# Kernel optimization log

Hardware: AMD Instinct MI355X
Metric: run time of the kernel (lower is better)

Reference implementation:

```python
import jax, jax.numpy as jnp
import numpy as np

N_NODES = 50000


def sage_conv(x, src, dst, Wl, bl, Wr):
    # mean-aggregate neighbor features: message from src -> dst
    msg = x[src]                                            # [E, d]
    agg = jax.ops.segment_sum(msg, dst, num_segments=N_NODES)
    deg = jax.ops.segment_sum(jnp.ones((src.shape[0],), x.dtype), dst,
                              num_segments=N_NODES)
    mean = agg / jnp.clip(deg, 1.0)[:, None]                # [N, d]
    # PyG SAGEConv: lin_l(mean) + lin_r(x); lin_l has bias, lin_r does not
    return mean @ Wl.T + bl + x @ Wr.T


def setup_inputs() -> dict:
    key = jax.random.key(0)
    ks = jax.random.split(key, 10)
    d_in, d_h = 128, 256
    E = 800000
    x = jax.random.normal(ks[0], (N_NODES, d_in), jnp.float32)
    edge_index = jax.random.randint(ks[1], (2, E), 0, N_NODES, jnp.int32)
    s = 0.05
    return {
        "x": x,
        "edge_index": edge_index,
        "W1_l": jax.random.normal(ks[2], (d_h, d_in), jnp.float32) * s,
        "b1": jax.random.normal(ks[3], (d_h,), jnp.float32) * s,
        "W1_r": jax.random.normal(ks[4], (d_h, d_in), jnp.float32) * s,
        "W2_l": jax.random.normal(ks[5], (d_h, d_h), jnp.float32) * s,
        "b2": jax.random.normal(ks[6], (d_h,), jnp.float32) * s,
        "W2_r": jax.random.normal(ks[7], (d_h, d_h), jnp.float32) * s,
        "head_w": jax.random.normal(ks[8], (1, d_h), jnp.float32) * s,
        "head_b": jax.random.normal(ks[9], (1,), jnp.float32) * s,
    }


def reference(x, edge_index, W1_l, b1, W1_r, W2_l, b2, W2_r, head_w, head_b):
    src, dst = edge_index[0], edge_index[1]
    h = jax.nn.relu(sage_conv(x, src, dst, W1_l, b1, W1_r))
    # dropout is identity in eval mode
    h = jax.nn.relu(sage_conv(h, src, dst, W2_l, b2, W2_r))
    out = h @ head_w.T + head_b                              # [N, 1]
    return out[:, 0]                                         # [N]
```

## Files before the change

kernel.cpp:

```cpp
#include <hip/hip_runtime.h>
#include <hip/hip_bf16.h>
#include <hip/hip_fp8.h>

#define D_IN 128
#define D_H  256
#define NBLK 128
#define BSH  7
#define BNODES 128

typedef __attribute__((ext_vector_type(8))) short short8;
typedef __attribute__((ext_vector_type(4))) float floatx4;

__device__ __forceinline__ unsigned short f2bf(float f) {
    __hip_bfloat16 h = __float2bfloat16(f);
    return *reinterpret_cast<unsigned short*>(&h);
}
__device__ __forceinline__ float bf2f(unsigned short s) {
    union { unsigned int u; float f; } v;
    v.u = ((unsigned int)s) << 16;
    return v.f;
}
__device__ __forceinline__ unsigned char f2fp8(float f) {
    __hip_fp8_e4m3 t(f);
    return (unsigned char)t.__x;
}

__global__ void p1_hist_conv_k(const int* __restrict__ dst, int* __restrict__ cnt2d,
                               int E, int NB,
                               const float* __restrict__ x, unsigned short* __restrict__ xb,
                               unsigned char* __restrict__ xb8, int nx4,
                               const float* __restrict__ w1l, unsigned short* __restrict__ w1lb,
                               const float* __restrict__ w1r, unsigned short* __restrict__ w1rb, int nw14,
                               const float* __restrict__ w2l, unsigned short* __restrict__ w2lb,
                               const float* __restrict__ w2r, unsigned short* __restrict__ w2rb, int nw24) {
    if (blockIdx.x < NBLK) {
        __shared__ int h[512];
        for (int i = threadIdx.x; i < NB; i += 256) h[i] = 0;
        __syncthreads();
        for (int e = blockIdx.x * 256 + threadIdx.x; e < E; e += NBLK * 256)
            atomicAdd(&h[dst[e] >> BSH], 1);
        __syncthreads();
        for (int i = threadIdx.x; i < NB; i += 256)
            cnt2d[blockIdx.x * NB + i] = h[i];
        return;
    }
    int i = (blockIdx.x - NBLK) * 256 + threadIdx.x;
    if (i < nx4) {
        float4 v = ((const float4*)x)[i];
        ushort4 u;
        u.x = f2bf(v.x); u.y = f2bf(v.y); u.z = f2bf(v.z); u.w = f2bf(v.w);
        ((ushort4*)xb)[i] = u;
        uchar4 c;
        c.x = f2fp8(v.x); c.y = f2fp8(v.y); c.z = f2fp8(v.z); c.w = f2fp8(v.w);
        ((uchar4*)xb8)[i] = c;
        return;
    }
    i -= nx4;
    const float* s; unsigned short* d; int k;
    if (i < nw14) { s = w1l; d = w1lb; k = i; }
    else {
        i -= nw14;
        if (i < nw14) { s = w1r; d = w1rb; k = i; }
        else {
            i -= nw14;
            if (i < nw24) { s = w2l; d = w2lb; k = i; }
            else {
                i -= nw24;
                if (i >= nw24) return;
                s = w2r; d = w2rb; k = i;
            }
        }
    }
    float4 v = ((const float4*)s)[k];
    ushort4 u;
    u.x = f2bf(v.x); u.y = f2bf(v.y); u.z = f2bf(v.z); u.w = f2bf(v.w);
    ((ushort4*)d)[k] = u;
}

__global__ __launch_bounds__(NBLK) void bucket_scan_k(const int* __restrict__ cnt2d,
                                                      int* __restrict__ off2d,
                                                      int* __restrict__ tot, int NB) {
    const int B = blockIdx.x, t = threadIdx.x;
    __shared__ int sc[NBLK];
    __shared__ int orig[NBLK];
    int v = cnt2d[t * NB + B];
    orig[t] = v; sc[t] = v;
    __syncthreads();
    for (int off = 1; off < NBLK; off <<= 1) {
        int u = (t >= off) ? sc[t - off] : 0;
        __syncthreads();
        sc[t] += u;
        __syncthreads();
    }
    off2d[t * NB + B] = sc[t] - orig[t];
    if (t == NBLK - 1) tot[B] = sc[t];
}

__global__ __launch_bounds__(512) void base_scan_k(const int* __restrict__ tot,
                                                   int* __restrict__ base,
                                                   int* __restrict__ rp,
                                                   int NB, int M, int E) {
    __shared__ int sc[512];
    const int t = threadIdx.x;
    int v = (t < NB) ? tot[t] : 0;
    sc[t] = v;
    __syncthreads();
    for (int off = 1; off < 512; off <<= 1) {
        int u = (t >= off) ? sc[t - off] : 0;
        __syncthreads();
        sc[t] += u;
        __syncthreads();
    }
    if (t < NB) base[t] = sc[t] - v;
    if (t == NB - 1) base[NB] = sc[t];
    if (t == 0) rp[M] = E;
}

__global__ __launch_bounds__(256) void place_k(const int* __restrict__ src,
                                               const int* __restrict__ dst,
                                               const int* __restrict__ off2d,
                                               const int* __restrict__ base,
                                               unsigned int* __restrict__ staging,
                                               int E, int NB) {
    __shared__ int cur[512];
    const int b = blockIdx.x;
    for (int i = threadIdx.x; i < NB; i += 256)
        cur[i] = base[i] + off2d[b * NB + i];
    __syncthreads();
    for (int e = b * 256 + threadIdx.x; e < E; e += NBLK * 256) {
        const int d = dst[e];
        const int pos = atomicAdd(&cur[d >> BSH], 1);
        staging[pos] = ((unsigned int)(d & (BNODES - 1)) << 16) | (unsigned int)src[e];
    }
}

__global__ __launch_bounds__(256) void bucket_sort_k(const unsigned int* __restrict__ staging,
                                                     const int* __restrict__ base,
                                                     int* __restrict__ rp, int* __restrict__ col,
                                                     int M) {
    const int B = blockIdx.x, tid = threadIdx.x;
    __shared__ int h[BNODES], sc[BNODES], cur[BNODES];
    if (tid < BNODES) h[tid] = 0;
    __syncthreads();
    const int s0 = base[B], s1 = base[B + 1];
    for (int i = s0 + tid; i < s1; i += 256)
        atomicAdd(&h[staging[i] >> 16], 1);
    __syncthreads();
    if (tid < BNODES) sc[tid] = h[tid];
    __syncthreads();
    for (int off = 1; off < BNODES; off <<= 1) {
        int v = 0;
        if (tid < BNODES && tid >= off) v = sc[tid - off];
        __syncthreads();
        if (tid < BNODES) sc[tid] += v;
        __syncthreads();
    }
    if (tid < BNODES) {
        const int excl = sc[tid] - h[tid];
        const int node = B * BNODES + tid;
        if (node < M) rp[node] = s0 + excl;
        cur[tid] = s0 + excl;
    }
    __syncthreads();
    for (int i = s0 + tid; i < s1; i += 256) {
        const unsigned int u = staging[i];
        const int pos = atomicAdd(&cur[u >> 16], 1);
        col[pos] = (int)(u & 0xFFFFu);
    }
}

template <int UNP>
__device__ __forceinline__ int agg1_stage(const unsigned char* __restrict__ X8,
                                          const int* __restrict__ col,
                                          int j, int e, int sel, int l32, float* acc) {
    for (; j + 2 * UNP <= e; j += 2 * UNP) {
        int c0[UNP], c1[UNP];
#pragma unroll
        for (int u = 0; u < UNP; ++u) { c0[u] = col[j + 2 * u]; c1[u] = col[j + 2 * u + 1]; }
        unsigned int vals[UNP];
#pragma unroll
        for (int u = 0; u < UNP; ++u) {
            const int cs = sel ? c1[u] : c0[u];
            vals[u] = *(const unsigned int*)(X8 + (size_t)cs * 128 + l32 * 4);
        }
#pragma unroll
        for (int u = 0; u < UNP; ++u) {
            __hip_fp8x4_e4m3 p;
            p.__x = vals[u];
            float4 f = (float4)p;
            acc[0] += f.x; acc[1] += f.y; acc[2] += f.z; acc[3] += f.w;
        }
    }
    return j;
}

__global__ __launch_bounds__(256) void aggregate1_k(
    const unsigned char* __restrict__ X8, const int* __restrict__ col,
    const int* __restrict__ rp, unsigned short* __restrict__ out, int Mnodes) {
    int node = __builtin_amdgcn_readfirstlane((blockIdx.x << 2) + (threadIdx.x >> 6));
    if (node >= Mnodes) return;
    const int lane = threadIdx.x & 63;
    const int sel = lane >> 5;
    const int l32 = lane & 31;
    const int s = rp[node], e = rp[node + 1];
    float acc[4] = {0.f, 0.f, 0.f, 0.f};

    int j = s;
    j = agg1_stage<4>(X8, col, j, e, sel, l32, acc);
    j = agg1_stage<2>(X8, col, j, e, sel, l32, acc);
    j = agg1_stage<1>(X8, col, j, e, sel, l32, acc);
    if (j < e) {
        const int c0 = col[j];
        if (sel == 0) {
            unsigned int v = *(const unsigned int*)(X8 + (size_t)c0 * 128 + l32 * 4);
            __hip_fp8x4_e4m3 p;
            p.__x = v;
            float4 f = (float4)p;
            acc[0] += f.x; acc[1] += f.y; acc[2] += f.z; acc[3] += f.w;
        }
    }
#pragma unroll
    for (int k = 0; k < 4; ++k) acc[k] += __shfl_xor(acc[k], 32, 64);
    const float inv = 1.f / fmaxf((float)(e - s), 1.f);
    if (sel == 0) {
        ushort4 o;
        o.x = f2bf(acc[0] * inv); o.y = f2bf(acc[1] * inv);
        o.z = f2bf(acc[2] * inv); o.w = f2bf(acc[3] * inv);
        *(ushort4*)(out + (size_t)node * 128 + l32 * 4) = o;
    }
}

template <int UN>
__device__ __forceinline__ int agg_stage_fp8(const unsigned char* __restrict__ X8,
                                             const int* __restrict__ col,
                                             int j, int e, int lane, float* acc) {
    for (; j + UN <= e; j += UN) {
        int cs[UN];
#pragma unroll
        for (int u = 0; u < UN; ++u) cs[u] = col[j + u];
        unsigned int vals[UN];
#pragma unroll
        for (int u = 0; u < UN; ++u)
            vals[u] = *(const unsigned int*)(X8 + (size_t)cs[u] * 256 + lane * 4);
#pragma unroll
        for (int u = 0; u < UN; ++u) {
            __hip_fp8x4_e4m3 p;
            p.__x = vals[u];
            float4 f = (float4)p;
            acc[0] += f.x; acc[1] += f.y; acc[2] += f.z; acc[3] += f.w;
        }
    }
    return j;
}

__global__ __launch_bounds__(256) void aggregate2_k(
    const unsigned char* __restrict__ X8, const int* __restrict__ col,
    const int* __restrict__ rp, unsigned short* __restrict__ out, int Mnodes) {
    int node = __builtin_amdgcn_readfirstlane((blockIdx.x << 2) + (threadIdx.x >> 6));
    if (node >= Mnodes) return;
    const int lane = threadIdx.x & 63;
    const int s = rp[node], e = rp[node + 1];
    float acc[4] = {0.f, 0.f, 0.f, 0.f};

    int j = s;
    j = agg_stage_fp8<8>(X8, col, j, e, lane, acc);
    j = agg_stage_fp8<4>(X8, col, j, e, lane, acc);
    j = agg_stage_fp8<2>(X8, col, j, e, lane, acc);
    j = agg_stage_fp8<1>(X8, col, j, e, lane, acc);

    const float inv = 1.f / fmaxf((float)(e - s), 1.f);
    ushort4 o;
    o.x = f2bf(acc[0] * inv); o.y = f2bf(acc[1] * inv);
    o.z = f2bf(acc[2] * inv); o.w = f2bf(acc[3] * inv);
    *(ushort4*)(out + (size_t)node * 256 + lane * 4) = o;
}

template <int K, bool HEAD>
__global__ __launch_bounds__(256, 2) void gemm_mfma_k(
    const unsigned short* __restrict__ A1, const unsigned short* __restrict__ W1,
    const unsigned short* __restrict__ A2, const unsigned short* __restrict__ W2,
    const float* __restrict__ bias, unsigned short* __restrict__ Hout,
    unsigned char* __restrict__ Hout8,
    const float* __restrict__ hw, const float* __restrict__ hb,
    float* __restrict__ out, int M) {
    __shared__ __align__(16) unsigned short sA[128 * 40];
    __shared__ __align__(16) unsigned short sB[256 * 40];
    __shared__ float head_acc[128];

    constexpr int NCK = K / 32;
    constexpr int NC = 2 * NCK;

    const int tid = threadIdx.x;
    const int wave = tid >> 6;
    const int lane = tid & 63;
    const int c = lane & 15;
    const int q = lane >> 4;
    const int m0 = blockIdx.x * 128;

    if (HEAD && tid < 128) head_acc[tid] = 0.f;

    floatx4 acc[8][4];
#pragma unroll
    for (int mi = 0; mi < 8; ++mi)
#pragma unroll
        for (int ni = 0; ni < 4; ++ni) acc[mi][ni] = (floatx4){0.f, 0.f, 0.f, 0.f};

    const int arow = tid >> 1;
    const int aseg = (tid & 1) * 16;
    const int brow = tid >> 2;
    const int bseg = (tid & 3) * 8;
    int gr = m0 + arow;
    if (gr >= M) gr = M - 1;

    auto loadChunk = [&](int t, short8& a0, short8& a1, short8* b) {
        const unsigned short* Ap = (t >= NCK) ? A2 : A1;
        const unsigned short* Wp = (t >= NCK) ? W2 : W1;
        const int k0 = (t & (NCK - 1)) * 32;
        a0 = *(const short8*)(Ap + (size_t)gr * K + k0 + aseg);
        a1 = *(const short8*)(Ap + (size_t)gr * K + k0 + aseg + 8);
#pragma unroll
        for (int i = 0; i < 4; ++i)
            b[i] = *(const short8*)(Wp + (size_t)(brow + i * 64) * K + k0 + bseg);
    };

    short8 ca0, ca1, cb[4], na0, na1, nb[4];
    loadChunk(0, ca0, ca1, cb);

#pragma unroll 1
    for (int t = 0; t < NC; ++t) {
        __syncthreads();
        *(short8*)&sA[arow * 40 + aseg] = ca0;
        *(short8*)&sA[arow * 40 + aseg + 8] = ca1;
#pragma unroll
        for (int i = 0; i < 4; ++i)
            *(short8*)&sB[(brow + i * 64) * 40 + bseg] = cb[i];
        if (t + 1 < NC)
            loadChunk(t + 1, na0, na1, nb);
        __syncthreads();

        short8 af[8], bf[4];
#pragma unroll
        for (int mi = 0; mi < 8; ++mi)
            af[mi] = *(const short8*)&sA[(mi * 16 + c) * 40 + q * 8];
#pragma unroll
        for (int ni = 0; ni < 4; ++ni)
            bf[ni] = *(const short8*)&sB[(wave * 64 + ni * 16 + c) * 40 + q * 8];
#pragma unroll
        for (int mi = 0; mi < 8; ++mi)
#pragma unroll
            for (int ni = 0; ni < 4; ++ni)
                acc[mi][ni] = __builtin_amdgcn_mfma_f32_16x16x32_bf16(
                    af[mi], bf[ni], acc[mi][ni], 0, 0, 0);

        ca0 = na0; ca1 = na1;
#pragma unroll
        for (int i = 0; i < 4; ++i) cb[i] = nb[i];
    }

    if (!HEAD) {
#pragma unroll
        for (int mi = 0; mi < 8; ++mi)
#pragma unroll
            for (int ni = 0; ni < 4; ++ni) {
                const int n = wave * 64 + ni * 16 + c;
                const float bv = bias[n];
#pragma unroll
                for (int reg = 0; reg < 4; ++reg) {
                    const int m = m0 + mi * 16 + q * 4 + reg;
                    if (m < M) {
                        float v = fmaxf(acc[mi][ni][reg] + bv, 0.f);
                        Hout[(size_t)m * 256 + n] = f2bf(v);
                        Hout8[(size_t)m * 256 + n] = f2fp8(v);
                    }
                }
            }
    } else {
#pragma unroll
        for (int mi = 0; mi < 8; ++mi) {
            float p[4] = {0.f, 0.f, 0.f, 0.f};
#pragma unroll
            for (int ni = 0; ni < 4; ++ni) {
                const int n = wave * 64 + ni * 16 + c;
                const float bv = bias[n];
                const float hv = hw[n];
#pragma unroll
                for (int reg = 0; reg < 4; ++reg)
                    p[reg] += fmaxf(acc[mi][ni][reg] + bv, 0.f) * hv;
            }
#pragma unroll
            for (int reg = 0; reg < 4; ++reg) {
                float v = p[reg];
                v += __shfl_xor(v, 1, 64);
                v += __shfl_xor(v, 2, 64);
                v += __shfl_xor(v, 4, 64);
                v += __shfl_xor(v, 8, 64);
                if (c == 0) atomicAdd(&head_acc[mi * 16 + q * 4 + reg], v);
            }
        }
        __syncthreads();
        if (tid < 128) {
            const int m = m0 + tid;
            if (m < M) out[m] = head_acc[tid] + hb[0];
        }
    }
}

extern "C" void kernel_launch(void* const* d_in, const int* in_sizes, int n_in,
                              void* d_out, int out_size, void* d_ws, size_t ws_size,
                              hipStream_t stream) {
    const float* x    = (const float*)d_in[0];
    const int*   ei   = (const int*)d_in[1];
    const float* W1l  = (const float*)d_in[2];
    const float* b1   = (const float*)d_in[3];
    const float* W1r  = (const float*)d_in[4];
    const float* W2l  = (const float*)d_in[5];
    const float* b2   = (const float*)d_in[6];
    const float* W2r  = (const float*)d_in[7];
    const float* hw   = (const float*)d_in[8];
    const float* hb   = (const float*)d_in[9];
    float* out = (float*)d_out;

    const int M = in_sizes[0] / D_IN;
    const int E = in_sizes[1] / 2;
    const int* src = ei;
    const int* dst = ei + E;
    const int NB = (M + BNODES - 1) / BNODES;

    size_t off = 0;
    auto alloc = [&](size_t bytes) -> void* {
        void* p = (char*)d_ws + off;
        off += (bytes + 255) & ~(size_t)255;
        return p;
    };
    int* cnt2d = (int*)alloc((size_t)NBLK * NB * 4);
    int* off2d = (int*)alloc((size_t)NBLK * NB * 4);
    int* tot   = (int*)alloc((size_t)NB * 4);
    int* base  = (int*)alloc((size_t)(NB + 1) * 4);
    unsigned int* staging = (unsigned int*)alloc((size_t)E * 4);
    int* rp    = (int*)alloc((size_t)(M + 1) * 4);
    int* col   = (int*)alloc((size_t)E * 4);
    unsigned short* xb    = (unsigned short*)alloc((size_t)M * D_IN * 2);
    unsigned char*  xb8   = (unsigned char*)alloc((size_t)M * D_IN);
    unsigned short* w1lb  = (unsigned short*)alloc((size_t)D_H * D_IN * 2);
    unsigned short* w1rb  = (unsigned short*)alloc((size_t)D_H * D_IN * 2);
    unsigned short* w2lb  = (unsigned short*)alloc((size_t)D_H * D_H * 2);
    unsigned short* w2rb  = (unsigned short*)alloc((size_t)D_H * D_H * 2);
    unsigned short* mean1 = (unsigned short*)alloc((size_t)M * D_IN * 2);
    unsigned short* h1    = (unsigned short*)alloc((size_t)M * D_H * 2);
    unsigned char*  h8    = (unsigned char*)alloc((size_t)M * D_H);
    unsigned short* mean2 = (unsigned short*)alloc((size_t)M * D_H * 2);

    const int nx4 = (M * D_IN) / 4;
    const int nw14 = (D_H * D_IN) / 4;
    const int nw24 = (D_H * D_H) / 4;
    const int tot4 = nx4 + 2 * nw14 + 2 * nw24;
    const int convblk = (tot4 + 255) / 256;
    p1_hist_conv_k<<<NBLK + convblk, 256, 0, stream>>>(
        dst, cnt2d, E, NB,
        x, xb, xb8, nx4, W1l, w1lb, W1r, w1rb, nw14, W2l, w2lb, W2r, w2rb, nw24);
    bucket_scan_k<<<NB, NBLK, 0, stream>>>(cnt2d, off2d, tot, NB);
    base_scan_k<<<1, 512, 0, stream>>>(tot, base, rp, NB, M, E);
    place_k<<<NBLK, 256, 0, stream>>>(src, dst, off2d, base, staging, E, NB);
    bucket_sort_k<<<NB, 256, 0, stream>>>(staging, base, rp, col, M);

    const int nblk = (M + 127) / 128;
    const int ablk = (M + 3) / 4;

    aggregate1_k<<<ablk, 256, 0, stream>>>(xb8, col, rp, mean1, M);
    gemm_mfma_k<D_IN, false><<<nblk, 256, 0, stream>>>(
        mean1, w1lb, xb, w1rb, b1, h1, h8, nullptr, nullptr, nullptr, M);

    aggregate2_k<<<ablk, 256, 0, stream>>>(h8, col, rp, mean2, M);
    gemm_mfma_k<D_H, true><<<nblk, 256, 0, stream>>>(
        mean2, w2lb, h1, w2rb, b2, nullptr, nullptr, hw, hb, out, M);
}
```

Baseline: 232.8 us.

## Stage scatter in LDS and drop separate base-scan kernel in CSR build

Each place block now owns a contiguous edge chunk, first sorts that chunk by bucket into LDS, then writes it to the global staging array in bucket runs. The scatter writes become mostly contiguous instead of random. The single-block base_scan kernel is removed: place_k rescans bucket totals itself, and bucket_sort_k recomputes its start offset by reducing the preceding totals. This saves one kernel launch and one serialization point, but adds redundant scans in every block and relies on the per-block chunk fitting in MAXCH entries of LDS.

```diff
diff --git a/kernel.cpp b/kernel.cpp
--- a/kernel.cpp
+++ b/kernel.cpp
@@ -7,6 +7,7 @@
 #define NBLK 128
 #define BSH  7
 #define BNODES 128
+#define MAXCH 6400
 
 typedef __attribute__((ext_vector_type(8))) short short8;
 typedef __attribute__((ext_vector_type(4))) float floatx4;
@@ -23,6 +24,25 @@
 __device__ __forceinline__ unsigned char f2fp8(float f) {
     __hip_fp8_e4m3 t(f);
     return (unsigned char)t.__x;
+}
+
+__device__ __forceinline__ void excl_scan512(int* vals, int NB, int* part) {
+    const int t = threadIdx.x;
+    const int i0 = t * 2, i1 = t * 2 + 1;
+    int v0 = (i0 < NB) ? vals[i0] : 0;
+    int v1 = (i1 < NB) ? vals[i1] : 0;
+    part[t] = v0 + v1;
+    __syncthreads();
+    for (int off = 1; off < 256; off <<= 1) {
+        int u = (t >= off) ? part[t - off] : 0;
+        __syncthreads();
+        part[t] += u;
+        __syncthreads();
+    }
+    const int pre = (t == 0) ? 0 : part[t - 1];
+    if (i0 < NB) vals[i0] = pre;
+    if (i1 < NB) vals[i1] = pre + v0;
+    __syncthreads();
 }
 
 __global__ void p1_hist_conv_k(const int* __restrict__ dst, int* __restrict__ cnt2d,
@@ -37,7 +57,10 @@
         __shared__ int h[512];
         for (int i = threadIdx.x; i < NB; i += 256) h[i] = 0;
         __syncthreads();
-        for (int e = blockIdx.x * 256 + threadIdx.x; e < E; e += NBLK * 256)
+        const int CH = (E + NBLK - 1) / NBLK;
+        const int e0 = blockIdx.x * CH;
+        const int e1 = min(e0 + CH, E);
+        for (int e = e0 + threadIdx.x; e < e1; e += 256)
             atomicAdd(&h[dst[e] >> BSH], 1);
         __syncthreads();
         for (int i = threadIdx.x; i < NB; i += 256)
@@ -96,55 +119,67 @@
     if (t == NBLK - 1) tot[B] = sc[t];
 }
 
-__global__ __launch_bounds__(512) void base_scan_k(const int* __restrict__ tot,
-                                                   int* __restrict__ base,
-                                                   int* __restrict__ rp,
-                                                   int NB, int M, int E) {
-    __shared__ int sc[512];
-    const int t = threadIdx.x;
-    int v = (t < NB) ? tot[t] : 0;
-    sc[t] = v;
-    __syncthreads();
-    for (int off = 1; off < 512; off <<= 1) {
-        int u = (t >= off) ? sc[t - off] : 0;
-        __syncthreads();
-        sc[t] += u;
-        __syncthreads();
-    }
-    if (t < NB) base[t] = sc[t] - v;
-    if (t == NB - 1) base[NB] = sc[t];
-    if (t == 0) rp[M] = E;
-}
-
 __global__ __launch_bounds__(256) void place_k(const int* __restrict__ src,
                                                const int* __restrict__ dst,
                                                const int* __restrict__ off2d,
-                                               const int* __restrict__ base,
+                                               const int* __restrict__ tot,
                                                unsigned int* __restrict__ staging,
                                                int E, int NB) {
-    __shared__ int cur[512];
-    const int b = blockIdx.x;
-    for (int i = threadIdx.x; i < NB; i += 256)
-        cur[i] = base[i] + off2d[b * NB + i];
-    __syncthreads();
-    for (int e = b * 256 + threadIdx.x; e < E; e += NBLK * 256) {
+    __shared__ unsigned int lstage[MAXCH];
+    __shared__ int lstart[512], lcur[512], runstart[512];
+    __shared__ int part[256];
+    const int b = blockIdx.x, tid = threadIdx.x;
+    const int CH = (E + NBLK - 1) / NBLK;
+    const int e0 = b * CH;
+    const int e1 = min(e0 + CH, E);
+    const int n = e1 - e0;
+
+    for (int i = tid; i < NB; i += 256) { lstart[i] = 0; runstart[i] = tot[i]; }
+    __syncthreads();
+    for (int e = e0 + tid; e < e1; e += 256)
+        atomicAdd(&lstart[dst[e] >> BSH], 1);
+    __syncthreads();
+    excl_scan512(lstart, NB, part);
+    excl_scan512(runstart, NB, part);
+    for (int i = tid; i < NB; i += 256) {
+        runstart[i] += off2d[b * NB + i];
+        lcur[i] = lstart[i];
+    }
+    __syncthreads();
+    for (int e = e0 + tid; e < e1; e += 256) {
         const int d = dst[e];
-        const int pos = atomicAdd(&cur[d >> BSH], 1);
-        staging[pos] = ((unsigned int)(d & (BNODES - 1)) << 16) | (unsigned int)src[e];
+        const int pos = atomicAdd(&lcur[d >> BSH], 1);
+        lstage[pos] = ((unsigned int)d << 16) | (unsigned int)src[e];
+    }
+    __syncthreads();
+    for (int i = tid; i < n; i += 256) {
+        const unsigned int u = lstage[i];
+        const int bkt = (int)(u >> (16 + BSH));
+        staging[runstart[bkt] + (i - lstart[bkt])] = u;
     }
 }
 
 __global__ __launch_bounds__(256) void bucket_sort_k(const unsigned int* __restrict__ staging,
-                                                     const int* __restrict__ base,
+                                                     const int* __restrict__ tot,
                                                      int* __restrict__ rp, int* __restrict__ col,
-                                                     int M) {
+                                                     int M, int NB) {
     const int B = blockIdx.x, tid = threadIdx.x;
+    __shared__ int red[256];
     __shared__ int h[BNODES], sc[BNODES], cur[BNODES];
+    __shared__ int s0s, s1s;
+    int acc = 0;
+    for (int i = tid; i < B; i += 256) acc += tot[i];
+    red[tid] = acc; __syncthreads();
+    for (int off = 128; off > 0; off >>= 1) {
+        if (tid < off) red[tid] += red[tid + off];
+        __syncthreads();
+    }
+    if (tid == 0) { s0s = red[0]; s1s = red[0] + tot[B]; }
     if (tid < BNODES) h[tid] = 0;
     __syncthreads();
-    const int s0 = base[B], s1 = base[B + 1];
+    const int s0 = s0s, s1 = s1s;
     for (int i = s0 + tid; i < s1; i += 256)
-        atomicAdd(&h[staging[i] >> 16], 1);
+        atomicAdd(&h[(staging[i] >> 16) & (BNODES - 1)], 1);
     __syncthreads();
     if (tid < BNODES) sc[tid] = h[tid];
     __syncthreads();
@@ -161,10 +196,11 @@
         if (node < M) rp[node] = s0 + excl;
         cur[tid] = s0 + excl;
     }
+    if (B == NB - 1 && tid == 0) rp[M] = s1;
     __syncthreads();
     for (int i = s0 + tid; i < s1; i += 256) {
         const unsigned int u = staging[i];
-        const int pos = atomicAdd(&cur[u >> 16], 1);
+        const int pos = atomicAdd(&cur[(u >> 16) & (BNODES - 1)], 1);
         col[pos] = (int)(u & 0xFFFFu);
     }
 }
@@ -435,7 +471,6 @@
     int* cnt2d = (int*)alloc((size_t)NBLK * NB * 4);
     int* off2d = (int*)alloc((size_t)NBLK * NB * 4);
     int* tot   = (int*)alloc((size_t)NB * 4);
-    int* base  = (int*)alloc((size_t)(NB + 1) * 4);
     unsigned int* staging = (unsigned int*)alloc((size_t)E * 4);
     int* rp    = (int*)alloc((size_t)(M + 1) * 4);
     int* col   = (int*)alloc((size_t)E * 4);
@@ -459,9 +494,8 @@
         dst, cnt2d, E, NB,
         x, xb, xb8, nx4, W1l, w1lb, W1r, w1rb, nw14, W2l, w2lb, W2r, w2rb, nw24);
     bucket_scan_k<<<NB, NBLK, 0, stream>>>(cnt2d, off2d, tot, NB);
-    base_scan_k<<<1, 512, 0, stream>>>(tot, base, rp, NB, M, E);
-    place_k<<<NBLK, 256, 0, stream>>>(src, dst, off2d, base, staging, E, NB);
-    bucket_sort_k<<<NB, 256, 0, stream>>>(staging, base, rp, col, M);
+    place_k<<<NBLK, 256, 0, stream>>>(src, dst, off2d, tot, staging, E, NB);
+    bucket_sort_k<<<NB, 256, 0, stream>>>(staging, tot, rp, col, M, NB);
 
     const int nblk = (M + 127) / 128;
     const int ablk = (M + 3) / 4;
```

Result: no change. 231.7 us (-0.5%).
